# Performance work log

Measured on AMD Instinct MI355X. Metric: run time of the kernel, lower is better.

The kernel has to match this reference:

```python
import jax, jax.numpy as jnp
import numpy as np
from jax import lax

C1, C2 = 64, 128
B, H2, W2 = 16, 64, 64
EPS = 1e-5


def conv2d(x, w, b, pad):
    y = lax.conv_general_dilated(x, w, (1, 1), [(pad, pad), (pad, pad)],
                                 dimension_numbers=('NCHW', 'OIHW', 'NCHW'))
    return y + b[None, :, None, None]


def batchnorm(x, g, be):
    # training-mode BN (batch statistics), matching torch nn.BatchNorm2d default
    m = jnp.mean(x, axis=(0, 2, 3), keepdims=True)
    v = jnp.var(x, axis=(0, 2, 3), keepdims=True)
    return (x - m) * jax.lax.rsqrt(v + EPS) * g[None, :, None, None] + be[None, :, None, None]


def up2_bilinear_ac(x):
    # bilinear upsample x2 with align_corners=True (nn.UpsamplingBilinear2d)
    b, c, h, w = x.shape
    yy = jnp.arange(2 * h, dtype=x.dtype) * ((h - 1) / (2 * h - 1))
    xx = jnp.arange(2 * w, dtype=x.dtype) * ((w - 1) / (2 * w - 1))
    y0 = jnp.floor(yy).astype(jnp.int32); y1 = jnp.minimum(y0 + 1, h - 1)
    x0 = jnp.floor(xx).astype(jnp.int32); x1 = jnp.minimum(x0 + 1, w - 1)
    wy = (yy - y0.astype(x.dtype))
    wx = (xx - x0.astype(x.dtype))
    rows = x[:, :, y0, :] * (1 - wy)[:, None] + x[:, :, y1, :] * wy[:, None]
    return rows[:, :, :, x0] * (1 - wx) + rows[:, :, :, x1] * wx


def dilate(x, k):
    # grayscale morphological dilation with kxk ones kernel == sliding-window max
    return lax.reduce_window(x, -jnp.inf, lax.max, (1, 1, k, k), (1, 1, 1, 1), 'SAME')


def pixel_shuffle2(x):
    b, c, h, w = x.shape
    x = x.reshape(b, c // 4, 2, 2, h, w)
    return x.transpose(0, 1, 4, 2, 5, 3).reshape(b, c // 4, 2 * h, 2 * w)


def setup_inputs() -> dict:
    key = jax.random.key(0)
    ks = jax.random.split(key, 16)
    s = 0.05
    d = {
        'cur_x': jax.random.normal(ks[0], (B, C1, 2 * H2, 2 * W2), jnp.float32),
        'dep_x': jax.random.normal(ks[1], (B, C2, H2, W2), jnp.float32),
        'in_map': jax.random.normal(ks[2], (B, 1, H2, W2), jnp.float32),
        'up_w': jax.random.normal(ks[3], (4 * C1, C2, 3, 3), jnp.float32) * s,
        'up_b': jnp.zeros((4 * C1,), jnp.float32),
        'up_g': jnp.ones((4 * C1,), jnp.float32),
        'up_be': jnp.zeros((4 * C1,), jnp.float32),
        'conv2_w': jax.random.normal(ks[4], (C1, C1, 3, 3), jnp.float32) * s,
        'conv2_b': jnp.zeros((C1,), jnp.float32),
        'beta': jnp.ones((1,), jnp.float32),
        'd1_w': jax.random.normal(ks[5], (C1, C1, 3, 3), jnp.float32) * s,
        'd1_b': jnp.zeros((C1,), jnp.float32),
        'd1_g': jnp.ones((C1,), jnp.float32),
        'd1_be': jnp.zeros((C1,), jnp.float32),
        'd2_w': jax.random.normal(ks[6], (C1, C1, 3, 3), jnp.float32) * s,
        'd2_b': jnp.zeros((C1,), jnp.float32),
        'd2_g': jnp.ones((C1,), jnp.float32),
        'd2_be': jnp.zeros((C1,), jnp.float32),
        'd3_w': jax.random.normal(ks[7], (C1, C1, 3, 3), jnp.float32) * s,
        'd3_b': jnp.zeros((C1,), jnp.float32),
        'd3_g': jnp.ones((C1,), jnp.float32),
        'd3_be': jnp.zeros((C1,), jnp.float32),
        'out_w': jax.random.normal(ks[8], (1, C1, 7, 7), jnp.float32) * s,
        'out_b': jnp.zeros((1,), jnp.float32),
    }
    return d


def reference(cur_x, dep_x, in_map, up_w, up_b, up_g, up_be, conv2_w, conv2_b, beta,
              d1_w, d1_b, d1_g, d1_be, d2_w, d2_b, d2_g, d2_be, d3_w, d3_b, d3_g, d3_be,
              out_w, out_b):
    # up: conv(C2 -> 4*C1) + BN + ReLU, then PixelShuffle(2)
    dep = jax.nn.relu(batchnorm(conv2d(dep_x, up_w, up_b, 1), up_g, up_be))
    dep = pixel_shuffle2(dep)                       # [B, C1, H, W]
    imap = jax.nn.sigmoid(up2_bilinear_ac(in_map))  # [B, 1, H, W]
    # focus_background: dilated(map) - map (increase_input_map is identity, sf=1)
    increase_map = dilate(imap, 3) - imap
    b_feature = cur_x * increase_map
    fn = conv2d(b_feature, conv2_w, conv2_b, 1)
    r = jax.nn.relu(batchnorm(conv2d(dep + beta * fn, d1_w, d1_b, 1), d1_g, d1_be))
    r = jax.nn.relu(batchnorm(conv2d(r, d2_w, d2_b, 1), d2_g, d2_be))
    r = jax.nn.relu(batchnorm(conv2d(r, d3_w, d3_b, 1), d3_g, d3_be))
    output_map = conv2d(r, out_w, out_b, 3)
    return (r, output_map)
```

## Files before the change

### kernel.cpp

```cpp
#include <hip/hip_runtime.h>
#include <hip/hip_bf16.h>

using bf16 = __hip_bfloat16;
typedef __attribute__((ext_vector_type(8))) short bfrag;
typedef __attribute__((ext_vector_type(4))) float ffrag;

__device__ __forceinline__ float b2f(bf16 v) { return __bfloat162float(v); }
__device__ __forceinline__ float ldin(const void* p, int i, int isbf) {
    return isbf ? b2f(((const bf16*)p)[i]) : ((const float*)p)[i];
}
__device__ __forceinline__ void split2(float v, unsigned short& h, unsigned short& l) {
    bf16 hb = __float2bfloat16(v);
    h = __bfloat16_as_ushort(hb);
    l = __bfloat16_as_ushort(__float2bfloat16(v - __bfloat162float(hb)));
}

__global__ void detect_kernel(const unsigned* __restrict__ x, int* __restrict__ flag)
{
    int tid = threadIdx.x;
    int cnt = 0;
    for (int i = tid; i < 256; i += 64) {
        unsigned e = (x[i] >> 7) & 0xFFu;
        cnt += (e >= 110u && e <= 135u) ? 1 : 0;
    }
#pragma unroll
    for (int off = 32; off > 0; off >>= 1) cnt += __shfl_down(cnt, off, 64);
    if (tid == 0) *flag = (cnt >= 128) ? 1 : 0;
}

__global__ void zero_accum_kernel(float* __restrict__ a)
{
    for (int i = threadIdx.x; i < 896; i += 256) a[i] = 0.f;
}

template<int CIN, int COUT>
__global__ __launch_bounds__(256)
void wsplit_kernel(const void* __restrict__ w, unsigned short* __restrict__ whi,
                   unsigned short* __restrict__ wlo, const int* __restrict__ flagp)
{
    constexpr int NCH = CIN / 32, NCOG = COUT / 16;
    constexpr int total = 9 * NCH * NCOG * 512;
    int isbf = *flagp;
    int o = blockIdx.x * 256 + threadIdx.x;
    if (o >= total) return;
    int j = o & 7;
    int l = (o >> 3) & 63;
    int fb = o >> 9;
    int cg = fb % NCOG;
    int t2 = fb / NCOG;
    int ch = t2 % NCH;
    int tap = t2 / NCH;
    int co = cg * 16 + (l & 15);
    int ci = ch * 32 + (l >> 4) * 8 + j;
    float v = ldin(w, (co * CIN + ci) * 9 + tap, isbf);
    unsigned short h, lo2;
    split2(v, h, lo2);
    whi[o] = h;
    wlo[o] = lo2;
}

template<int CIN, int COUT, int H, int W, int TH,
         bool EXTIN, bool SMAP, bool EPI, bool BNIN, bool STATS>
__global__ __launch_bounds__(256, 2)
void conv3_mfma(const void* __restrict__ in,
                const unsigned short* __restrict__ whi,
                const unsigned short* __restrict__ wlo,
                const void* __restrict__ bias,
                const float* __restrict__ imapF,
                const float* __restrict__ dep,
                const void* __restrict__ betap,
                const float* __restrict__ accum,
                const void* __restrict__ bng, const void* __restrict__ bnbe,
                float* __restrict__ out, const int* __restrict__ flagp,
                float* __restrict__ sacc, int statC)
{
    constexpr int NCH  = CIN / 32;
    constexpr int NCOG = COUT / 16;
    constexpr int W2   = W + 2;
    constexpr int NP   = (TH + 2) * W2;
    constexpr int NPs  = NP + 1;
    constexpr int NE   = 4 * NP;

    __shared__ int4 s_hi[4 * NPs];
    __shared__ int4 s_lo[4 * NPs];
    __shared__ float s_ss[128];
    __shared__ float s_sm[SMAP ? NP : 1];
    __shared__ float s_st[STATS ? 2 : 1][4][64];

    const int isbf = *flagp;
    const bool skiplo = EXTIN && !SMAP && isbf;
    const int tid  = threadIdx.x;
    const int r0   = blockIdx.x * TH;
    const int bimg = r0 / H;
    const int y0im = bimg * H;
    const int coB  = blockIdx.y;

    if (BNIN) {
        if (tid < CIN) {
            const float n = (float)(16 * H * W);
            float S = accum[tid], S2 = accum[CIN + tid];
            float m = S / n;
            float var = fmaxf(S2 / n - m * m, 0.f);
            float scv = ldin(bng, tid, isbf) * rsqrtf(var + 1e-5f);
            s_ss[2 * tid]     = scv;
            s_ss[2 * tid + 1] = ldin(bnbe, tid, isbf) - m * scv;
        }
    }
    if (SMAP) {
        const float* ip = imapF + ((size_t)bimg << 14);
        for (int i = tid; i < NP; i += 256) {
            int rr = i / W2, cc = i - rr * W2;
            int gy = r0 - 1 + rr, gx = cc - 1;
            float sm = 0.f;
            if (gy >= y0im && gy < y0im + H && (unsigned)gx < (unsigned)W) {
                int y = gy - y0im;
                float ctr = ip[(y << 7) + gx];
                float mx = ctr;
#pragma unroll
                for (int dy = -1; dy <= 1; dy++) {
                    int yy = y + dy;
                    if ((unsigned)yy < 128u) {
#pragma unroll
                        for (int dx = -1; dx <= 1; dx++) {
                            int xx = gx + dx;
                            if ((unsigned)xx < 128u) mx = fmaxf(mx, ip[(yy << 7) + xx]);
                        }
                    }
                }
                sm = mx - ctr;
            }
            s_sm[i] = sm;
        }
    }

    const int lane = tid & 63;
    const int wv = tid >> 6;
    const int lx = lane & 15;
    const int gq = lane >> 4;

    ffrag acc[4][4];
#pragma unroll
    for (int mf = 0; mf < 4; mf++)
#pragma unroll
        for (int nf = 0; nf < 4; nf++) acc[mf][nf] = ffrag{0.f, 0.f, 0.f, 0.f};

    for (int ch = 0; ch < NCH; ch++) {
        const int c0 = ch * 32;
        __syncthreads();
        for (int e = tid; e < NE; e += 256) {
            int gg, pixin;
            if (EXTIN) { gg = e / NP; pixin = e - gg * NP; }
            else       { gg = e & 3;  pixin = e >> 2; }
            int rr = pixin / W2;
            int cc2 = pixin - rr * W2;
            int gy = r0 - 1 + rr;
            int gx = cc2 - 1;
            float v[8];
            bool ok = (gy >= y0im) && (gy < y0im + H) && ((unsigned)gx < (unsigned)W);
            if (ok) {
                if (EXTIN) {
                    int y = gy - y0im;
                    float sm = SMAP ? s_sm[pixin] : 1.f;
#pragma unroll
                    for (int j = 0; j < 8; j++) {
                        int gi = ((bimg * CIN + c0 + 8 * gg + j) * H + y) * W + gx;
                        v[j] = ldin(in, gi, isbf) * sm;
                    }
                } else {
                    const float* up = (const float*)in +
                        ((size_t)gy * W + gx) * CIN + c0 + 8 * gg;
                    float4 q0 = *(const float4*)up;
                    float4 q1 = *(const float4*)(up + 4);
                    v[0] = q0.x; v[1] = q0.y; v[2] = q0.z; v[3] = q0.w;
                    v[4] = q1.x; v[5] = q1.y; v[6] = q1.z; v[7] = q1.w;
                    if (BNIN) {
#pragma unroll
                        for (int j = 0; j < 8; j++) {
                            int chn = c0 + 8 * gg + j;
                            v[j] = fmaxf(fmaf(v[j], s_ss[2 * chn], s_ss[2 * chn + 1]), 0.f);
                        }
                    }
                }
            } else {
#pragma unroll
                for (int j = 0; j < 8; j++) v[j] = 0.f;
            }
            unsigned hp[4], lp[4];
#pragma unroll
            for (int j2 = 0; j2 < 4; j2++) {
                bf16 h0b = __float2bfloat16(v[2 * j2]);
                bf16 h1b = __float2bfloat16(v[2 * j2 + 1]);
                hp[j2] = (unsigned)__bfloat16_as_ushort(h0b) |
                         ((unsigned)__bfloat16_as_ushort(h1b) << 16);
                if (!skiplo) {
                    unsigned short l0 = __bfloat16_as_ushort(
                        __float2bfloat16(v[2 * j2] - b2f(h0b)));
                    unsigned short l1 = __bfloat16_as_ushort(
                        __float2bfloat16(v[2 * j2 + 1] - b2f(h1b)));
                    lp[j2] = (unsigned)l0 | ((unsigned)l1 << 16);
                }
            }
            s_hi[gg * NPs + pixin] = make_int4(hp[0], hp[1], hp[2], hp[3]);
            if (!skiplo)
                s_lo[gg * NPs + pixin] = make_int4(lp[0], lp[1], lp[2], lp[3]);
        }
        __syncthreads();
#pragma unroll
        for (int tap = 0; tap < 9; tap++) {
            const int ky = tap / 3, kx = tap % 3;
            bfrag ah[4];
#pragma unroll
            for (int mf = 0; mf < 4; mf++) {
                int p = 64 * wv + 16 * mf;
                int rI = p / W + ky;
                int cI = (p & (W - 1)) + kx + lx;
                int pix = rI * W2 + cI;
                ah[mf] = ((const bfrag*)s_hi)[gq * NPs + pix];
            }
            bfrag bh[4];
#pragma unroll
            for (int nf = 0; nf < 4; nf++) {
                int fb = (tap * NCH + ch) * NCOG + coB * 4 + nf;
                bh[nf] = ((const bfrag*)(whi + (size_t)fb * 512))[lane];
            }
#pragma unroll
            for (int nf = 0; nf < 4; nf++)
#pragma unroll
                for (int mf = 0; mf < 4; mf++)
                    acc[mf][nf] = __builtin_amdgcn_mfma_f32_16x16x32_bf16(
                        ah[mf], bh[nf], acc[mf][nf], 0, 0, 0);
            if (!skiplo) {
                bfrag al[4];
#pragma unroll
                for (int mf = 0; mf < 4; mf++) {
                    int p = 64 * wv + 16 * mf;
                    int rI = p / W + ky;
                    int cI = (p & (W - 1)) + kx + lx;
                    int pix = rI * W2 + cI;
                    al[mf] = ((const bfrag*)s_lo)[gq * NPs + pix];
                }
#pragma unroll
                for (int nf = 0; nf < 4; nf++)
#pragma unroll
                    for (int mf = 0; mf < 4; mf++)
                        acc[mf][nf] = __builtin_amdgcn_mfma_f32_16x16x32_bf16(
                            al[mf], bh[nf], acc[mf][nf], 0, 0, 0);
            }
            if (!isbf) {
                bfrag ah2[4];
#pragma unroll
                for (int mf = 0; mf < 4; mf++) {
                    int p = 64 * wv + 16 * mf;
                    int rI = p / W + ky;
                    int cI = (p & (W - 1)) + kx + lx;
                    int pix = rI * W2 + cI;
                    ah2[mf] = ((const bfrag*)s_hi)[gq * NPs + pix];
                }
                bfrag bl[4];
#pragma unroll
                for (int nf = 0; nf < 4; nf++) {
                    int fb = (tap * NCH + ch) * NCOG + coB * 4 + nf;
                    bl[nf] = ((const bfrag*)(wlo + (size_t)fb * 512))[lane];
                }
#pragma unroll
                for (int nf = 0; nf < 4; nf++)
#pragma unroll
                    for (int mf = 0; mf < 4; mf++)
                        acc[mf][nf] = __builtin_amdgcn_mfma_f32_16x16x32_bf16(
                            ah2[mf], bl[nf], acc[mf][nf], 0, 0, 0);
            }
        }
    }
    const float beta = EPI ? ldin(betap, 0, isbf) : 0.f;
    float sl[4] = {0.f, 0.f, 0.f, 0.f}, s2l[4] = {0.f, 0.f, 0.f, 0.f};
#pragma unroll
    for (int nf = 0; nf < 4; nf++) {
        int co = coB * 64 + nf * 16 + lx;
        float bi = ldin(bias, co, isbf);
#pragma unroll
        for (int mf = 0; mf < 4; mf++) {
#pragma unroll
            for (int r2 = 0; r2 < 4; r2++) {
                int p = 64 * wv + 16 * mf + gq * 4 + r2;
                int grow = r0 + p / W;
                int gcol = p & (W - 1);
                size_t oi = ((size_t)grow * W + gcol) * COUT + co;
                float vo = acc[mf][nf][r2] + bi;
                if (EPI) vo = dep[oi] + beta * vo;
                out[oi] = vo;
                if (STATS) {
                    sl[nf] += vo;
                    s2l[nf] = fmaf(vo, vo, s2l[nf]);
                }
            }
        }
    }
    if (STATS) {
#pragma unroll
        for (int nf = 0; nf < 4; nf++) {
            float s = sl[nf], q = s2l[nf];
            s += __shfl_xor(s, 16, 64); s += __shfl_xor(s, 32, 64);
            q += __shfl_xor(q, 16, 64); q += __shfl_xor(q, 32, 64);
            if (gq == 0) {
                s_st[0][wv][nf * 16 + lx] = s;
                s_st[1][wv][nf * 16 + lx] = q;
            }
        }
        __syncthreads();
        if (tid < 128) {
            int which = tid >> 6, c = tid & 63;
            float v = s_st[which][0][c] + s_st[which][1][c] +
                      s_st[which][2][c] + s_st[which][3][c];
            atomicAdd(&sacc[which * statC + coB * 64 + c], v);
        }
    }
}

__global__ __launch_bounds__(256)
void shuffle_bn_nhwc_kernel(const float* __restrict__ u, const float* __restrict__ accum,
                            const void* __restrict__ g, const void* __restrict__ be,
                            float* __restrict__ dep, const int* __restrict__ flagp)
{
    int isbf = *flagp;
    int tid = threadIdx.x;
    int c = tid & 63, ps = tid >> 6;
    float sc[4], sh[4];
#pragma unroll
    for (int q = 0; q < 4; q++) {
        int chn = 4 * c + q;
        float S = accum[chn], S2 = accum[256 + chn];
        const float n = 65536.f;
        float m = S / n;
        float var = fmaxf(S2 / n - m * m, 0.f);
        sc[q] = ldin(g, chn, isbf) * rsqrtf(var + 1e-5f);
        sh[q] = ldin(be, chn, isbf) - m * sc[q];
    }
    for (int sp = blockIdx.x * 4 + ps; sp < 65536; sp += gridDim.x * 4) {
        float4 q4 = *(const float4*)(u + (size_t)sp * 256 + 4 * c);
        float vals[4] = {q4.x, q4.y, q4.z, q4.w};
        int b = sp >> 12, rem = sp & 4095, y2 = rem >> 6, x2 = rem & 63;
#pragma unroll
        for (int dy = 0; dy < 2; dy++)
#pragma unroll
            for (int dx = 0; dx < 2; dx++) {
                int q = 2 * dy + dx;
                float v = fmaxf(fmaf(vals[q], sc[q], sh[q]), 0.f);
                size_t op = (size_t)(b * 128 + 2 * y2 + dy) * 128 + (2 * x2 + dx);
                dep[op * 64 + c] = v;
            }
    }
}

__global__ __launch_bounds__(256)
void imap_kernel(const void* __restrict__ im, float* __restrict__ imap,
                 const int* __restrict__ flagp)
{
    int isbf = *flagp;
    int idx = blockIdx.x * 256 + threadIdx.x;
    int x = idx & 127, y = (idx >> 7) & 127, b = idx >> 14;
    const float s = (float)(63.0 / 127.0);
    float yy = y * s, xx = x * s;
    int y0 = (int)yy, x0 = (int)xx;
    float wy = yy - y0, wx = xx - x0;
    int y1 = min(y0 + 1, 63), x1 = min(x0 + 1, 63);
    int base = b << 12;
    float v00 = ldin(im, base + (y0 << 6) + x0, isbf);
    float v01 = ldin(im, base + (y0 << 6) + x1, isbf);
    float v10 = ldin(im, base + (y1 << 6) + x0, isbf);
    float v11 = ldin(im, base + (y1 << 6) + x1, isbf);
    float r0 = v00 * (1.f - wy) + v10 * wy;
    float r1 = v01 * (1.f - wy) + v11 * wy;
    float v = r0 * (1.f - wx) + r1 * wx;
    imap[idx] = 1.f / (1.f + expf(-v));
}

__global__ __launch_bounds__(256)
void bn_out_kernel(const float* __restrict__ u, const float* __restrict__ accum,
                   const void* __restrict__ g, const void* __restrict__ be,
                   float* __restrict__ r3, void* __restrict__ dout,
                   const int* __restrict__ flagp)
{
    int isbf = *flagp;
    int tid = threadIdx.x;
    int c = tid & 63, ps = tid >> 6;
    float S = accum[c], S2 = accum[64 + c];
    const float n = 262144.f;
    float m = S / n;
    float var = fmaxf(S2 / n - m * m, 0.f);
    float sc = ldin(g, c, isbf) * rsqrtf(var + 1e-5f);
    float sh = ldin(be, c, isbf) - m * sc;
    __shared__ float s[64][65];
    int pix0 = blockIdx.x * 64;
#pragma unroll
    for (int ii = 0; ii < 16; ii++) {
        int p = ps + 4 * ii;
        float v = u[(size_t)(pix0 + p) * 64 + c];
        s[p][c] = fmaxf(fmaf(v, sc, sh), 0.f);
    }
    __syncthreads();
    int x = c;
    int row = pix0 >> 7, col0 = pix0 & 127;
    int b = row >> 7, y = row & 127;
#pragma unroll
    for (int jj = 0; jj < 16; jj++) {
        int cc = ps + 4 * jj;
        float v = s[x][cc];
        size_t oi = (((size_t)(b * 64 + cc)) << 14) + (y << 7) + col0 + x;
        r3[oi] = v;
        if (isbf) ((bf16*)dout)[oi] = __float2bfloat16(v);
        else      ((float*)dout)[oi] = v;
    }
}

__global__ __launch_bounds__(256, 2)
void conv7x7_part_kernel(const float* __restrict__ r, const void* __restrict__ w,
                         float* __restrict__ outP, const int* __restrict__ flagp)
{
    __shared__ float s_in[4][70][22];
    __shared__ float s_w[16][49];
    const int isbf = *flagp;
    int tid = threadIdx.x;
    int tx = tid & 15, ty = tid >> 4;
    int x0 = blockIdx.x * 16, y0 = blockIdx.y * 64;
    int b = blockIdx.z >> 2, g = blockIdx.z & 3;
    for (int i = tid; i < 16 * 49; i += 256) {
        int ci = i / 49, k = i - ci * 49;
        s_w[ci][k] = ldin(w, (g * 16 + ci) * 49 + k, isbf);
    }
    float acc[4] = {0.f, 0.f, 0.f, 0.f};

    for (int c0 = 0; c0 < 16; c0 += 4) {
        __syncthreads();
        for (int i = tid; i < 4 * 70 * 22; i += 256) {
            int ci = i / (70 * 22);
            int rem = i - ci * (70 * 22);
            int rr = rem / 22, cc = rem - rr * 22;
            int gy = y0 + rr - 3, gx = x0 + cc - 3;
            float v = 0.f;
            if ((unsigned)gy < 128u && (unsigned)gx < 128u)
                v = r[((b * 64 + g * 16 + c0 + ci) << 14) + (gy << 7) + gx];
            s_in[ci][rr][cc] = v;
        }
        __syncthreads();
        for (int ci = 0; ci < 4; ci++) {
            float wr[49];
#pragma unroll
            for (int k = 0; k < 49; k++) wr[k] = s_w[c0 + ci][k];
#pragma unroll
            for (int rr = 0; rr < 10; rr++) {
                float row[7];
#pragma unroll
                for (int c = 0; c < 7; c++) row[c] = s_in[ci][4 * ty + rr][tx + c];
#pragma unroll
                for (int oy = 0; oy < 4; oy++) {
                    int ky = rr - oy;
                    if (ky >= 0 && ky <= 6) {
#pragma unroll
                        for (int kx = 0; kx < 7; kx++)
                            acc[oy] = fmaf(row[kx], wr[ky * 7 + kx], acc[oy]);
                    }
                }
            }
        }
    }
#pragma unroll
    for (int oy = 0; oy < 4; oy++) {
        int y = y0 + 4 * ty + oy;
        outP[(g << 18) + (b << 14) + (y << 7) + x0 + tx] = acc[oy];
    }
}

__global__ __launch_bounds__(256)
void finalize_out_kernel(const float* __restrict__ outP, const void* __restrict__ bias,
                         void* __restrict__ outv, const int* __restrict__ flagp)
{
    int isbf = *flagp;
    int i = blockIdx.x * 256 + threadIdx.x;
    float bi = ldin(bias, 0, isbf);
    float v = (outP[i] + outP[i + 262144]) +
              (outP[i + 2 * 262144] + outP[i + 3 * 262144]) + bi;
    int oidx = 16777216 + i;
    if (isbf) ((bf16*)outv)[oidx] = __float2bfloat16(v);
    else      ((float*)outv)[oidx] = v;
}

extern "C" void kernel_launch(void* const* d_in, const int* in_sizes, int n_in,
                              void* d_out, int out_size, void* d_ws, size_t ws_size,
                              hipStream_t stream)
{
    (void)in_sizes; (void)n_in; (void)out_size; (void)ws_size;

    const void* cur_x   = d_in[0];
    const void* dep_x   = d_in[1];
    const void* in_map  = d_in[2];
    const void* up_w    = d_in[3];
    const void* up_b    = d_in[4];
    const void* up_g    = d_in[5];
    const void* up_be   = d_in[6];
    const void* conv2_w = d_in[7];
    const void* conv2_b = d_in[8];
    const void* beta    = d_in[9];
    const void* d1_w = d_in[10];
    const void* d1_b = d_in[11];
    const void* d1_g = d_in[12];
    const void* d1_be = d_in[13];
    const void* d2_w = d_in[14];
    const void* d2_b = d_in[15];
    const void* d2_g = d_in[16];
    const void* d2_be = d_in[17];
    const void* d3_w = d_in[18];
    const void* d3_b = d_in[19];
    const void* d3_g = d_in[20];
    const void* d3_be = d_in[21];
    const void* out_w = d_in[22];
    const void* out_b = d_in[23];

    char* ws = (char*)d_ws;
    float* W0    = (float*)ws;
    float* W1    = (float*)(ws + 67108864);
    float* accum = (float*)(ws + 134217728);
    int*   flag  = (int*)(ws + 134221824);
    float* a0 = accum;
    float* a1 = accum + 512;
    float* a2 = accum + 640;
    float* a3 = accum + 768;

    char* sc = (char*)d_out;
    unsigned short* whi1  = (unsigned short*)sc;
    unsigned short* wlo1  = whi1 + 294912;
    unsigned short* whi2  = wlo1 + 294912;
    unsigned short* wlo2  = whi2 + 36864;
    unsigned short* whiD1 = wlo2 + 36864;
    unsigned short* wloD1 = whiD1 + 36864;
    unsigned short* whiD2 = wloD1 + 36864;
    unsigned short* wloD2 = whiD2 + 36864;
    unsigned short* whiD3 = wloD2 + 36864;
    unsigned short* wloD3 = whiD3 + 36864;
    float* imapF = (float*)(sc + 1769472);

    detect_kernel<<<1, 64, 0, stream>>>((const unsigned*)cur_x, flag);
    zero_accum_kernel<<<1, 256, 0, stream>>>(accum);
    wsplit_kernel<128, 256><<<1152, 256, 0, stream>>>(up_w, whi1, wlo1, flag);
    wsplit_kernel<64, 64><<<144, 256, 0, stream>>>(conv2_w, whi2, wlo2, flag);
    wsplit_kernel<64, 64><<<144, 256, 0, stream>>>(d1_w, whiD1, wloD1, flag);
    wsplit_kernel<64, 64><<<144, 256, 0, stream>>>(d2_w, whiD2, wloD2, flag);
    wsplit_kernel<64, 64><<<144, 256, 0, stream>>>(d3_w, whiD3, wloD3, flag);

    conv3_mfma<128, 256, 64, 64, 4, true, false, false, false, true>
        <<<dim3(256, 4), 256, 0, stream>>>(dep_x, whi1, wlo1, up_b,
            nullptr, nullptr, nullptr, nullptr, nullptr, nullptr, W0, flag, a0, 256);
    imap_kernel<<<1024, 256, 0, stream>>>(in_map, imapF, flag);
    shuffle_bn_nhwc_kernel<<<2048, 256, 0, stream>>>(W0, a0, up_g, up_be, W1, flag);
    conv3_mfma<64, 64, 128, 128, 2, true, true, true, false, false>
        <<<dim3(1024, 1), 256, 0, stream>>>(cur_x, whi2, wlo2, conv2_b,
            imapF, W1, beta, nullptr, nullptr, nullptr, W0, flag, nullptr, 0);
    conv3_mfma<64, 64, 128, 128, 2, false, false, false, false, true>
        <<<dim3(1024, 1), 256, 0, stream>>>(W0, whiD1, wloD1, d1_b,
            nullptr, nullptr, nullptr, nullptr, nullptr, nullptr, W1, flag, a1, 64);
    conv3_mfma<64, 64, 128, 128, 2, false, false, false, true, true>
        <<<dim3(1024, 1), 256, 0, stream>>>(W1, whiD2, wloD2, d2_b,
            nullptr, nullptr, nullptr, a1, d1_g, d1_be, W0, flag, a2, 64);
    conv3_mfma<64, 64, 128, 128, 2, false, false, false, true, true>
        <<<dim3(1024, 1), 256, 0, stream>>>(W0, whiD3, wloD3, d3_b,
            nullptr, nullptr, nullptr, a2, d2_g, d2_be, W1, flag, a3, 64);
    bn_out_kernel<<<4096, 256, 0, stream>>>(W1, a3, d3_g, d3_be, W0, d_out, flag);
    conv7x7_part_kernel<<<dim3(8, 2, 64), 256, 0, stream>>>(W0, out_w, W1, flag);
    finalize_out_kernel<<<1024, 256, 0, stream>>>(W1, out_b, d_out, flag);
}
```

Before: 832.0 us.

## Retile conv kernels by column halves and pre-split dep_x into NHWC bf16 planes

Adds a pre-pass that transposes dep_x to NHWC and splits it into hi/lo bf16 planes, so the first conv loads pre-split int4 fragments instead of doing strided NCHW loads and conversion. The 128-wide convs are now tiled into 64-column halves with waves split across output channels (WCO=2). This halves per-block shared-memory staging and doubles the grid, and launch bounds raise minimum occupancy to 3–4 blocks per CU. The cost is an extra transpose kernel and pass over memory, more halo overlap, and fewer accumulators per wave.

```diff
diff --git a/kernel.cpp b/kernel.cpp
--- a/kernel.cpp
+++ b/kernel.cpp
@@ -59,9 +59,34 @@
     wlo[o] = lo2;
 }
 
-template<int CIN, int COUT, int H, int W, int TH,
-         bool EXTIN, bool SMAP, bool EPI, bool BNIN, bool STATS>
-__global__ __launch_bounds__(256, 2)
+__global__ __launch_bounds__(256)
+void dep_nhwc_kernel(const void* __restrict__ in, unsigned short* __restrict__ outp,
+                     const int* __restrict__ flagp)
+{
+    __shared__ unsigned short s_h[64][65];
+    __shared__ unsigned short s_l[64][65];
+    const int isbf = *flagp;
+    const int pb = blockIdx.x, cb = blockIdx.y, b = blockIdx.z;
+    for (int i = threadIdx.x; i < 4096; i += 256) {
+        int ci = i >> 6, pi = i & 63;
+        float v = ldin(in, ((b * 128 + cb * 64 + ci) << 12) + (pb << 6) + pi, isbf);
+        unsigned short h, l;
+        split2(v, h, l);
+        s_h[ci][pi] = h;
+        if (!isbf) s_l[ci][pi] = l;
+    }
+    __syncthreads();
+    for (int i = threadIdx.x; i < 4096; i += 256) {
+        int ci = i & 63, pi = i >> 6;
+        size_t o = ((size_t)(b * 4096 + pb * 64 + pi) << 7) + cb * 64 + ci;
+        outp[o] = s_h[ci][pi];
+        if (!isbf) outp[8388608 + o] = s_l[ci][pi];
+    }
+}
+
+template<int CIN, int COUT, int H, int W, int ROWS, int WCO, int MODE,
+         bool SMAP, bool EPI, bool BNIN, bool STATS, int MINW>
+__global__ __launch_bounds__(256, MINW)
 void conv3_mfma(const void* __restrict__ in,
                 const unsigned short* __restrict__ whi,
                 const unsigned short* __restrict__ wlo,
@@ -76,21 +101,26 @@
 {
     constexpr int NCH  = CIN / 32;
     constexpr int NCOG = COUT / 16;
-    constexpr int W2   = W + 2;
-    constexpr int NP   = (TH + 2) * W2;
+    constexpr int NCT  = W / 64;
+    constexpr int W2h  = 66;
+    constexpr int NP   = (ROWS + 2) * W2h;
     constexpr int NPs  = NP + 1;
     constexpr int NE   = 4 * NP;
+    constexpr int NF   = (64 / WCO) / 16;
+    constexpr int STCO = 64 / WCO;
+    constexpr size_t PLANE = (size_t)16 * H * W * CIN;
 
     __shared__ int4 s_hi[4 * NPs];
     __shared__ int4 s_lo[4 * NPs];
-    __shared__ float s_ss[128];
+    __shared__ float s_ss[BNIN ? 128 : 1];
     __shared__ float s_sm[SMAP ? NP : 1];
-    __shared__ float s_st[STATS ? 2 : 1][4][64];
+    __shared__ float s_st[STATS ? 2 : 1][4][STCO];
 
     const int isbf = *flagp;
-    const bool skiplo = EXTIN && !SMAP && isbf;
+    const bool uselo = !(isbf && (MODE == 2 || (MODE == 1 && !SMAP)));
     const int tid  = threadIdx.x;
-    const int r0   = blockIdx.x * TH;
+    const int r0   = (blockIdx.x / NCT) * ROWS;
+    const int x0   = (blockIdx.x % NCT) * 64;
     const int bimg = r0 / H;
     const int y0im = bimg * H;
     const int coB  = blockIdx.y;
@@ -109,8 +139,8 @@
     if (SMAP) {
         const float* ip = imapF + ((size_t)bimg << 14);
         for (int i = tid; i < NP; i += 256) {
-            int rr = i / W2, cc = i - rr * W2;
-            int gy = r0 - 1 + rr, gx = cc - 1;
+            int rr = i / W2h, cc = i - rr * W2h;
+            int gy = r0 - 1 + rr, gx = x0 - 1 + cc;
             float sm = 0.f;
             if (gy >= y0im && gy < y0im + H && (unsigned)gx < (unsigned)W) {
                 int y = gy - y0im;
@@ -135,74 +165,86 @@
 
     const int lane = tid & 63;
     const int wv = tid >> 6;
+    const int wpx = wv / WCO, wco = wv % WCO;
     const int lx = lane & 15;
     const int gq = lane >> 4;
 
-    ffrag acc[4][4];
+    ffrag acc[4][NF];
 #pragma unroll
     for (int mf = 0; mf < 4; mf++)
 #pragma unroll
-        for (int nf = 0; nf < 4; nf++) acc[mf][nf] = ffrag{0.f, 0.f, 0.f, 0.f};
+        for (int nf = 0; nf < NF; nf++) acc[mf][nf] = ffrag{0.f, 0.f, 0.f, 0.f};
 
     for (int ch = 0; ch < NCH; ch++) {
         const int c0 = ch * 32;
         __syncthreads();
         for (int e = tid; e < NE; e += 256) {
             int gg, pixin;
-            if (EXTIN) { gg = e / NP; pixin = e - gg * NP; }
-            else       { gg = e & 3;  pixin = e >> 2; }
-            int rr = pixin / W2;
-            int cc2 = pixin - rr * W2;
+            if (MODE == 1) { gg = e / NP; pixin = e - gg * NP; }
+            else           { gg = e & 3;  pixin = e >> 2; }
+            int rr = pixin / W2h;
+            int cc2 = pixin - rr * W2h;
             int gy = r0 - 1 + rr;
-            int gx = cc2 - 1;
-            float v[8];
+            int gx = x0 - 1 + cc2;
             bool ok = (gy >= y0im) && (gy < y0im + H) && ((unsigned)gx < (unsigned)W);
-            if (ok) {
-                if (EXTIN) {
-                    int y = gy - y0im;
-                    float sm = SMAP ? s_sm[pixin] : 1.f;
-#pragma unroll
-                    for (int j = 0; j < 8; j++) {
-                        int gi = ((bimg * CIN + c0 + 8 * gg + j) * H + y) * W + gx;
-                        v[j] = ldin(in, gi, isbf) * sm;
+            if (MODE == 2) {
+                int4 hv = make_int4(0, 0, 0, 0), lv = make_int4(0, 0, 0, 0);
+                if (ok) {
+                    size_t eb = (size_t)(gy * W + gx) * CIN + c0 + 8 * gg;
+                    hv = *(const int4*)((const unsigned short*)in + eb);
+                    if (!isbf) lv = *(const int4*)((const unsigned short*)in + PLANE + eb);
+                }
+                s_hi[gg * NPs + pixin] = hv;
+                if (!isbf) s_lo[gg * NPs + pixin] = lv;
+            } else {
+                float v[8];
+                if (ok) {
+                    if (MODE == 1) {
+                        int y = gy - y0im;
+                        float sm = SMAP ? s_sm[pixin] : 1.f;
+#pragma unroll
+                        for (int j = 0; j < 8; j++) {
+                            int gi = ((bimg * CIN + c0 + 8 * gg + j) * H + y) * W + gx;
+                            v[j] = ldin(in, gi, isbf) * sm;
+                        }
+                    } else {
+                        const float* up = (const float*)in +
+                            ((size_t)gy * W + gx) * CIN + c0 + 8 * gg;
+                        float4 q0 = *(const float4*)up;
+                        float4 q1 = *(const float4*)(up + 4);
+                        v[0] = q0.x; v[1] = q0.y; v[2] = q0.z; v[3] = q0.w;
+                        v[4] = q1.x; v[5] = q1.y; v[6] = q1.z; v[7] = q1.w;
+                        if (BNIN) {
+#pragma unroll
+                            for (int j = 0; j < 8; j++) {
+                                int chn = c0 + 8 * gg + j;
+                                v[j] = fmaxf(fmaf(v[j], s_ss[2 * chn], s_ss[2 * chn + 1]), 0.f);
+                            }
+                        }
                     }
                 } else {
-                    const float* up = (const float*)in +
-                        ((size_t)gy * W + gx) * CIN + c0 + 8 * gg;
-                    float4 q0 = *(const float4*)up;
-                    float4 q1 = *(const float4*)(up + 4);
-                    v[0] = q0.x; v[1] = q0.y; v[2] = q0.z; v[3] = q0.w;
-                    v[4] = q1.x; v[5] = q1.y; v[6] = q1.z; v[7] = q1.w;
-                    if (BNIN) {
-#pragma unroll
-                        for (int j = 0; j < 8; j++) {
-                            int chn = c0 + 8 * gg + j;
-                            v[j] = fmaxf(fmaf(v[j], s_ss[2 * chn], s_ss[2 * chn + 1]), 0.f);
-                        }
+#pragma unroll
+                    for (int j = 0; j < 8; j++) v[j] = 0.f;
+                }
+                unsigned hp[4], lp[4];
+#pragma unroll
+                for (int j2 = 0; j2 < 4; j2++) {
+                    bf16 h0b = __float2bfloat16(v[2 * j2]);
+                    bf16 h1b = __float2bfloat16(v[2 * j2 + 1]);
+                    hp[j2] = (unsigned)__bfloat16_as_ushort(h0b) |
+                             ((unsigned)__bfloat16_as_ushort(h1b) << 16);
+                    if (uselo) {
+                        unsigned short l0 = __bfloat16_as_ushort(
+                            __float2bfloat16(v[2 * j2] - b2f(h0b)));
+                        unsigned short l1 = __bfloat16_as_ushort(
+                            __float2bfloat16(v[2 * j2 + 1] - b2f(h1b)));
+                        lp[j2] = (unsigned)l0 | ((unsigned)l1 << 16);
                     }
                 }
-            } else {
-#pragma unroll
-                for (int j = 0; j < 8; j++) v[j] = 0.f;
-            }
-            unsigned hp[4], lp[4];
-#pragma unroll
-            for (int j2 = 0; j2 < 4; j2++) {
-                bf16 h0b = __float2bfloat16(v[2 * j2]);
-                bf16 h1b = __float2bfloat16(v[2 * j2 + 1]);
-                hp[j2] = (unsigned)__bfloat16_as_ushort(h0b) |
-                         ((unsigned)__bfloat16_as_ushort(h1b) << 16);
-                if (!skiplo) {
-                    unsigned short l0 = __bfloat16_as_ushort(
-                        __float2bfloat16(v[2 * j2] - b2f(h0b)));
-                    unsigned short l1 = __bfloat16_as_ushort(
-                        __float2bfloat16(v[2 * j2 + 1] - b2f(h1b)));
-                    lp[j2] = (unsigned)l0 | ((unsigned)l1 << 16);
-                }
-            }
-            s_hi[gg * NPs + pixin] = make_int4(hp[0], hp[1], hp[2], hp[3]);
-            if (!skiplo)
-                s_lo[gg * NPs + pixin] = make_int4(lp[0], lp[1], lp[2], lp[3]);
+                s_hi[gg * NPs + pixin] = make_int4(hp[0], hp[1], hp[2], hp[3]);
+                if (uselo)
+                    s_lo[gg * NPs + pixin] = make_int4(lp[0], lp[1], lp[2], lp[3]);
+            }
         }
         __syncthreads();
 #pragma unroll
@@ -211,36 +253,36 @@
             bfrag ah[4];
 #pragma unroll
             for (int mf = 0; mf < 4; mf++) {
-                int p = 64 * wv + 16 * mf;
-                int rI = p / W + ky;
-                int cI = (p & (W - 1)) + kx + lx;
-                int pix = rI * W2 + cI;
+                int p = 64 * wpx + 16 * mf;
+                int rI = (p >> 6) + ky;
+                int cI = (p & 63) + kx + lx;
+                int pix = rI * W2h + cI;
                 ah[mf] = ((const bfrag*)s_hi)[gq * NPs + pix];
             }
-            bfrag bh[4];
-#pragma unroll
-            for (int nf = 0; nf < 4; nf++) {
-                int fb = (tap * NCH + ch) * NCOG + coB * 4 + nf;
+            bfrag bh[NF];
+#pragma unroll
+            for (int nf = 0; nf < NF; nf++) {
+                int fb = (tap * NCH + ch) * NCOG + coB * 4 + wco * NF + nf;
                 bh[nf] = ((const bfrag*)(whi + (size_t)fb * 512))[lane];
             }
 #pragma unroll
-            for (int nf = 0; nf < 4; nf++)
+            for (int nf = 0; nf < NF; nf++)
 #pragma unroll
                 for (int mf = 0; mf < 4; mf++)
                     acc[mf][nf] = __builtin_amdgcn_mfma_f32_16x16x32_bf16(
                         ah[mf], bh[nf], acc[mf][nf], 0, 0, 0);
-            if (!skiplo) {
+            if (uselo) {
                 bfrag al[4];
 #pragma unroll
                 for (int mf = 0; mf < 4; mf++) {
-                    int p = 64 * wv + 16 * mf;
-                    int rI = p / W + ky;
-                    int cI = (p & (W - 1)) + kx + lx;
-                    int pix = rI * W2 + cI;
+                    int p = 64 * wpx + 16 * mf;
+                    int rI = (p >> 6) + ky;
+                    int cI = (p & 63) + kx + lx;
+                    int pix = rI * W2h + cI;
                     al[mf] = ((const bfrag*)s_lo)[gq * NPs + pix];
                 }
 #pragma unroll
-                for (int nf = 0; nf < 4; nf++)
+                for (int nf = 0; nf < NF; nf++)
 #pragma unroll
                     for (int mf = 0; mf < 4; mf++)
                         acc[mf][nf] = __builtin_amdgcn_mfma_f32_16x16x32_bf16(
@@ -250,20 +292,20 @@
                 bfrag ah2[4];
 #pragma unroll
                 for (int mf = 0; mf < 4; mf++) {
-                    int p = 64 * wv + 16 * mf;
-                    int rI = p / W + ky;
-                    int cI = (p & (W - 1)) + kx + lx;
-                    int pix = rI * W2 + cI;
+                    int p = 64 * wpx + 16 * mf;
+                    int rI = (p >> 6) + ky;
+                    int cI = (p & 63) + kx + lx;
+                    int pix = rI * W2h + cI;
                     ah2[mf] = ((const bfrag*)s_hi)[gq * NPs + pix];
                 }
-                bfrag bl[4];
-#pragma unroll
-                for (int nf = 0; nf < 4; nf++) {
-                    int fb = (tap * NCH + ch) * NCOG + coB * 4 + nf;
+                bfrag bl[NF];
+#pragma unroll
+                for (int nf = 0; nf < NF; nf++) {
+                    int fb = (tap * NCH + ch) * NCOG + coB * 4 + wco * NF + nf;
                     bl[nf] = ((const bfrag*)(wlo + (size_t)fb * 512))[lane];
                 }
 #pragma unroll
-                for (int nf = 0; nf < 4; nf++)
+                for (int nf = 0; nf < NF; nf++)
 #pragma unroll
                     for (int mf = 0; mf < 4; mf++)
                         acc[mf][nf] = __builtin_amdgcn_mfma_f32_16x16x32_bf16(
@@ -272,18 +314,20 @@
         }
     }
     const float beta = EPI ? ldin(betap, 0, isbf) : 0.f;
-    float sl[4] = {0.f, 0.f, 0.f, 0.f}, s2l[4] = {0.f, 0.f, 0.f, 0.f};
-#pragma unroll
-    for (int nf = 0; nf < 4; nf++) {
-        int co = coB * 64 + nf * 16 + lx;
+    float sl[NF], s2l[NF];
+#pragma unroll
+    for (int nf = 0; nf < NF; nf++) { sl[nf] = 0.f; s2l[nf] = 0.f; }
+#pragma unroll
+    for (int nf = 0; nf < NF; nf++) {
+        int co = coB * 64 + wco * STCO + nf * 16 + lx;
         float bi = ldin(bias, co, isbf);
 #pragma unroll
         for (int mf = 0; mf < 4; mf++) {
 #pragma unroll
             for (int r2 = 0; r2 < 4; r2++) {
-                int p = 64 * wv + 16 * mf + gq * 4 + r2;
-                int grow = r0 + p / W;
-                int gcol = p & (W - 1);
+                int p = 64 * wpx + 16 * mf + gq * 4 + r2;
+                int grow = r0 + (p >> 6);
+                int gcol = x0 + (p & 63);
                 size_t oi = ((size_t)grow * W + gcol) * COUT + co;
                 float vo = acc[mf][nf][r2] + bi;
                 if (EPI) vo = dep[oi] + beta * vo;
@@ -297,7 +341,7 @@
     }
     if (STATS) {
 #pragma unroll
-        for (int nf = 0; nf < 4; nf++) {
+        for (int nf = 0; nf < NF; nf++) {
             float s = sl[nf], q = s2l[nf];
             s += __shfl_xor(s, 16, 64); s += __shfl_xor(s, 32, 64);
             q += __shfl_xor(q, 16, 64); q += __shfl_xor(q, 32, 64);
@@ -309,8 +353,14 @@
         __syncthreads();
         if (tid < 128) {
             int which = tid >> 6, c = tid & 63;
-            float v = s_st[which][0][c] + s_st[which][1][c] +
-                      s_st[which][2][c] + s_st[which][3][c];
+            float v;
+            if (WCO == 1) {
+                v = s_st[which][0][c] + s_st[which][1][c] +
+                    s_st[which][2][c] + s_st[which][3][c];
+            } else {
+                int wc = c >> 5, ci = c & 31;
+                v = s_st[which][wc][ci] + s_st[which][2 + wc][ci];
+            }
             atomicAdd(&sacc[which * statC + coB * 64 + c], v);
         }
     }
@@ -545,23 +595,25 @@
     wsplit_kernel<64, 64><<<144, 256, 0, stream>>>(d1_w, whiD1, wloD1, flag);
     wsplit_kernel<64, 64><<<144, 256, 0, stream>>>(d2_w, whiD2, wloD2, flag);
     wsplit_kernel<64, 64><<<144, 256, 0, stream>>>(d3_w, whiD3, wloD3, flag);
-
-    conv3_mfma<128, 256, 64, 64, 4, true, false, false, false, true>
-        <<<dim3(256, 4), 256, 0, stream>>>(dep_x, whi1, wlo1, up_b,
+    dep_nhwc_kernel<<<dim3(64, 2, 16), 256, 0, stream>>>(
+        dep_x, (unsigned short*)W1, flag);
+
+    conv3_mfma<128, 256, 64, 64, 4, 1, 2, false, false, false, true, 3>
+        <<<dim3(256, 4), 256, 0, stream>>>((const void*)W1, whi1, wlo1, up_b,
             nullptr, nullptr, nullptr, nullptr, nullptr, nullptr, W0, flag, a0, 256);
     imap_kernel<<<1024, 256, 0, stream>>>(in_map, imapF, flag);
     shuffle_bn_nhwc_kernel<<<2048, 256, 0, stream>>>(W0, a0, up_g, up_be, W1, flag);
-    conv3_mfma<64, 64, 128, 128, 2, true, true, true, false, false>
-        <<<dim3(1024, 1), 256, 0, stream>>>(cur_x, whi2, wlo2, conv2_b,
+    conv3_mfma<64, 64, 128, 128, 2, 2, 1, true, true, false, false, 4>
+        <<<dim3(2048, 1), 256, 0, stream>>>(cur_x, whi2, wlo2, conv2_b,
             imapF, W1, beta, nullptr, nullptr, nullptr, W0, flag, nullptr, 0);
-    conv3_mfma<64, 64, 128, 128, 2, false, false, false, false, true>
-        <<<dim3(1024, 1), 256, 0, stream>>>(W0, whiD1, wloD1, d1_b,
+    conv3_mfma<64, 64, 128, 128, 2, 2, 0, false, false, false, true, 4>
+        <<<dim3(2048, 1), 256, 0, stream>>>(W0, whiD1, wloD1, d1_b,
             nullptr, nullptr, nullptr, nullptr, nullptr, nullptr, W1, flag, a1, 64);
-    conv3_mfma<64, 64, 128, 128, 2, false, false, false, true, true>
-        <<<dim3(1024, 1), 256, 0, stream>>>(W1, whiD2, wloD2, d2_b,
+    conv3_mfma<64, 64, 128, 128, 2, 2, 0, false, false, true, true, 4>
+        <<<dim3(2048, 1), 256, 0, stream>>>(W1, whiD2, wloD2, d2_b,
             nullptr, nullptr, nullptr, a1, d1_g, d1_be, W0, flag, a2, 64);
-    conv3_mfma<64, 64, 128, 128, 2, false, false, false, true, true>
-        <<<dim3(1024, 1), 256, 0, stream>>>(W0, whiD3, wloD3, d3_b,
+    conv3_mfma<64, 64, 128, 128, 2, 2, 0, false, false, true, true, 4>
+        <<<dim3(2048, 1), 256, 0, stream>>>(W0, whiD3, wloD3, d3_b,
             nullptr, nullptr, nullptr, a2, d2_g, d2_be, W1, flag, a3, 64);
     bn_out_kernel<<<4096, 256, 0, stream>>>(W1, a3, d3_g, d3_be, W0, d_out, flag);
     conv7x7_part_kernel<<<dim3(8, 2, 64), 256, 0, stream>>>(W0, out_w, W1, flag);
```

Result: faster. 798.1 us (-4.1%).
